# Kernel optimization log

Hardware: AMD Instinct MI355X
Metric: run time of the kernel (lower is better)

## Reference

```python
import jax, jax.numpy as jnp
import numpy as np
from jax import lax

WIN = 15      # sliding window size
BINS = 64     # luminance histogram bins
ALPHA = 0.9   # local vs global histogram mix
LAM1 = 0.5    # a-channel (material) removal weight
LAM2 = 0.5    # b-channel (material) removal weight
EPS = 1e-6


def _box_sum(x, win):
    return lax.reduce_window(x, 0.0, lax.add, (1, win, win, 1), (1, 1, 1, 1), 'SAME')


def setup_inputs() -> dict:
    key = jax.random.key(0)
    u = jax.random.uniform(key, (4, 3, 512, 512), dtype=jnp.float32)
    L = u[:, 0] * 100.0                 # L in [0,100]
    a = u[:, 1] * 255.0 - 128.0         # a in [-128,127]
    b = u[:, 2] * 255.0 - 128.0         # b in [-128,127]
    return {"batch_lab_raw": jnp.stack([L, a, b], axis=1)}


def reference(batch_lab_raw):
    # Normalize channels
    Ln = jnp.clip(batch_lab_raw[:, 0] / 100.0, 0.0, 1.0)      # (B,H,W)
    an = (batch_lab_raw[:, 1] + 128.0) / 255.0                # (B,H,W)
    bn = (batch_lab_raw[:, 2] + 128.0) / 255.0                # (B,H,W)

    # --- windowed luminance histogram anomaly ---
    idx = jnp.clip((Ln * BINS).astype(jnp.int32), 0, BINS - 1)            # (B,H,W)
    onehot = jax.nn.one_hot(idx, BINS, dtype=Ln.dtype)                    # (B,H,W,K)
    cnt = _box_sum(onehot, WIN)                                           # (B,H,W,K)
    n = _box_sum(jnp.ones(Ln.shape + (1,), Ln.dtype), WIN)                # (B,H,W,1) valid-pixel count
    # probability of own bin within local window
    p_loc = jnp.take_along_axis(cnt / n, idx[..., None], axis=-1)[..., 0]  # (B,H,W)
    # global per-image histogram probability of own bin
    p_glob_bins = jnp.mean(onehot, axis=(1, 2))                            # (B,K)
    p_glob = jnp.einsum('bhwk,bk->bhw', onehot, p_glob_bins)              # (B,H,W)

    S = -jnp.log(ALPHA * p_loc + (1.0 - ALPHA) * p_glob + EPS)            # surprise
    S_min = jnp.min(S, axis=(1, 2), keepdims=True)
    S_max = jnp.max(S, axis=(1, 2), keepdims=True)
    L_anom_norm = (S - S_min) / (S_max - S_min + EPS)                     # (B,H,W)

    # --- de-materialized illumination: remove local chroma (material) variation ---
    mu_a = _box_sum(an[..., None], WIN)[..., 0] / n[..., 0]
    mu_b = _box_sum(bn[..., None], WIN)[..., 0] / n[..., 0]
    L_perp = jnp.clip(Ln - LAM1 * (an - mu_a) - LAM2 * (bn - mu_b), 0.0, 1.0)

    return (L_perp[:, None], L_anom_norm[:, None])  # each (B,1,H,W)
```

## Files before the change

kernel.cpp:

```cpp
#include <hip/hip_runtime.h>

#define Hh 512
#define Ww 512
#define NPIX (Hh*Ww)
#define BATCH 4


__global__ __launch_bounds__(256) void k_hist(const float* __restrict__ in,
                                              unsigned* __restrict__ hp) {
    __shared__ unsigned lh[64];
    const int tid = threadIdx.x;
    if (tid < 64) lh[tid] = 0u;
    __syncthreads();
    const int img = blockIdx.x >> 6, sub = blockIdx.x & 63;
    const float4* Lp = (const float4*)(in + (size_t)img * 3 * NPIX) + sub * 1024;
    #pragma unroll
    for (int t = 0; t < 4; ++t) {
        float4 v = Lp[t*256 + tid];
        float f[4] = {v.x, v.y, v.z, v.w};
        #pragma unroll
        for (int j = 0; j < 4; ++j) {
            float ln = fminf(fmaxf(f[j] / 100.0f, 0.0f), 1.0f);
            int idx = min((int)(ln * 64.0f), 63);
            atomicAdd(&lh[idx], 1u);
        }
    }
    __syncthreads();
    if (tid < 64) hp[((size_t)img*64 + tid)*64 + sub] = lh[tid];
}

__global__ __launch_bounds__(256, 8) void k_main(const float* __restrict__ in,
        const unsigned* __restrict__ hp, float* __restrict__ bmin,
        float* __restrict__ bmax, float* __restrict__ out)
{
    __shared__ unsigned s_pk[46*9];
    __shared__ float s_c[46*36];
    __shared__ float s_cc[32*33];
    __shared__ float s_lnc[32*16];
    __shared__ float lhf[64];
    __shared__ float red[8];

    const int tx = threadIdx.x, ty = threadIdx.y;
    const int tid = ty*16 + tx;
    const int bx = blockIdx.x * 16, by = blockIdx.y * 32;
    const int img = blockIdx.z;
    const float* Lp = in + (size_t)img * 3 * NPIX;

    {
        const int bin = tid >> 2, grp = tid & 3;
        const uint4* p = (const uint4*)(hp + ((size_t)img*64 + bin)*64 + grp*16);
        uint4 x0 = p[0], x1 = p[1], x2 = p[2], x3 = p[3];
        unsigned sum = x0.x+x0.y+x0.z+x0.w + x1.x+x1.y+x1.z+x1.w
                     + x2.x+x2.y+x2.z+x2.w + x3.x+x3.y+x3.z+x3.w;
        sum += __shfl_xor(sum, 1);
        sum += __shfl_xor(sum, 2);
        if (grp == 0) lhf[bin] = (float)sum * (1.0f/262144.0f);
    }

    const int s = tx + 1;
    const int j0 = s >> 2;
    const unsigned m20 = 0x7FFFu << (s & 3);
    unsigned wm[5];
    #pragma unroll
    for (int i = 0; i < 5; ++i) {
        unsigned n = (m20 >> (4*i)) & 0xFu;
        wm[i] = (n&1u)*0x80u | (n&2u)*0x4000u | (n&4u)*0x200000u | (n&8u)*0x10000000u;
    }

    float4 Lv[2], Av[2], Bv[2];
    bool vld[2];
    #pragma unroll
    for (int it = 0; it < 2; ++it) {
        const int l = tid + it*256;
        const int r = l >> 3, c4 = l & 7;
        const int gy = by - 7 + r, gx0 = bx - 8 + c4*4;
        vld[it] = (l < 368) && gy >= 0 && gy < Hh && gx0 >= 0 && gx0 < Ww;
        if (vld[it]) {
            const int g = gy*Ww + gx0;
            Lv[it] = *(const float4*)(Lp + g);
            Av[it] = *(const float4*)(Lp + NPIX + g);
            Bv[it] = *(const float4*)(Lp + 2*NPIX + g);
        }
    }
    #pragma unroll
    for (int it = 0; it < 2; ++it) {
        const int l = tid + it*256;
        if (l < 368) {
            const int r = l >> 3, c4 = l & 7;
            unsigned pk = 0x7F7F7F7Fu;
            float4 cv = {0.f, 0.f, 0.f, 0.f};
            if (vld[it]) {
                const float l0 = fminf(fmaxf(Lv[it].x / 100.0f, 0.0f), 1.0f);
                const float l1 = fminf(fmaxf(Lv[it].y / 100.0f, 0.0f), 1.0f);
                const float l2 = fminf(fmaxf(Lv[it].z / 100.0f, 0.0f), 1.0f);
                const float l3 = fminf(fmaxf(Lv[it].w / 100.0f, 0.0f), 1.0f);
                const int b0 = min((int)(l0*64.0f), 63), b1 = min((int)(l1*64.0f), 63);
                const int b2 = min((int)(l2*64.0f), 63), b3 = min((int)(l3*64.0f), 63);
                pk = (unsigned)b0 | ((unsigned)b1<<8) | ((unsigned)b2<<16) | ((unsigned)b3<<24);
                const float k255 = 1.0f/255.0f;
                cv.x = (Av[it].x+128.0f)*k255 + (Bv[it].x+128.0f)*k255;
                cv.y = (Av[it].y+128.0f)*k255 + (Bv[it].y+128.0f)*k255;
                cv.z = (Av[it].z+128.0f)*k255 + (Bv[it].z+128.0f)*k255;
                cv.w = (Av[it].w+128.0f)*k255 + (Bv[it].w+128.0f)*k255;
                if (r >= 7 && r < 39 && c4 >= 2 && c4 <= 5) {
                    float4 lv4 = {l0, l1, l2, l3};
                    *(float4*)&s_lnc[(r-7)*16 + 4*(c4-2)] = lv4;
                }
            }
            s_pk[r*9 + c4] = pk;
            *(float4*)&s_c[r*36 + c4*4] = cv;
        }
    }
    __syncthreads();

    for (int l = tid; l < 512; l += 256) {
        const int q = l >> 5, c = l & 31;
        float mid = 0.f;
        #pragma unroll
        for (int k = 1; k < 15; ++k) mid += s_c[(2*q+k)*36 + c];
        s_cc[(2*q)*33 + c]   = mid + s_c[(2*q)*36 + c];
        s_cc[(2*q+1)*33 + c] = mid + s_c[(2*q+15)*36 + c];
    }
    __syncthreads();

    const int r0 = 2*ty;
    const int cbyte = tx + 8;
    const unsigned cb0 = (s_pk[(r0+7)*9 + (cbyte>>2)] >> (8*(cbyte&3))) & 0xFFu;
    const unsigned cb1 = (s_pk[(r0+8)*9 + (cbyte>>2)] >> (8*(cbyte&3))) & 0xFFu;
    const unsigned cb40 = cb0 * 0x01010101u;
    const unsigned cb41 = cb1 * 0x01010101u;
    const unsigned K = 0x7F7F7F7Fu;
    int a0 = 0, a1 = 0, a2 = 0, a3 = 0;
    const unsigned* rp = s_pk + r0*9 + j0;

    #pragma unroll
    for (int k = 0; k < 16; ++k) {
        const unsigned d0 = rp[k*9+0], d1 = rp[k*9+1], d2 = rp[k*9+2],
                       d3 = rp[k*9+3], d4 = rp[k*9+4];
        if (k != 15) {
            a0 += __popc(~((d0^cb40)+K) & wm[0]);
            a1 += __popc(~((d1^cb40)+K) & wm[1]);
            a0 += __popc(~((d2^cb40)+K) & wm[2]);
            a1 += __popc(~((d3^cb40)+K) & wm[3]);
            a0 += __popc(~((d4^cb40)+K) & wm[4]);
        }
        if (k != 0) {
            a2 += __popc(~((d0^cb41)+K) & wm[0]);
            a3 += __popc(~((d1^cb41)+K) & wm[1]);
            a2 += __popc(~((d2^cb41)+K) & wm[2]);
            a3 += __popc(~((d3^cb41)+K) & wm[3]);
            a2 += __popc(~((d4^cb41)+K) & wm[4]);
        }
    }
    const int c0 = a0 + a1, c1 = a2 + a3;

    float sc0 = 0.f, sc1 = 0.f;
    const float* ccp = s_cc + r0*33 + s;
    #pragma unroll
    for (int dx = 0; dx < 15; ++dx) { sc0 += ccp[dx]; sc1 += ccp[33+dx]; }

    const int gx = bx + tx;
    const int gy0 = by + r0;
    const int cols  = min(gx+7, Ww-1) - max(gx-7, 0) + 1;
    const int rows0 = min(gy0+7, Hh-1) - max(gy0-7, 0) + 1;
    const int rows1 = min(gy0+8, Hh-1) - max(gy0-6, 0) + 1;
    const float inv0 = __builtin_amdgcn_rcpf((float)(rows0*cols));
    const float inv1 = __builtin_amdgcn_rcpf((float)(rows1*cols));
    const float pg0 = lhf[cb0];
    const float pg1 = lhf[cb1];
    const float S0 = -__logf(0.9f*((float)c0*inv0) + 0.1f*pg0 + 1e-6f);
    const float S1 = -__logf(0.9f*((float)c1*inv1) + 0.1f*pg1 + 1e-6f);
    const int gbase = img*NPIX + gy0*Ww + gx;

    const float lp0 = s_lnc[r0*16 + tx]     - 0.5f*(s_c[(r0+7)*36 + tx+8] - sc0*inv0);
    const float lp1 = s_lnc[(r0+1)*16 + tx] - 0.5f*(s_c[(r0+8)*36 + tx+8] - sc1*inv1);
    out[gbase]      = fminf(fmaxf(lp0, 0.f), 1.f);
    out[gbase + Ww] = fminf(fmaxf(lp1, 0.f), 1.f);
    float* outN = out + (size_t)BATCH*NPIX;
    outN[gbase]      = S0;
    outN[gbase + Ww] = S1;

    float smin = fminf(S0, S1), smax = fmaxf(S0, S1);
    #pragma unroll
    for (int off = 32; off >= 1; off >>= 1) {
        smin = fminf(smin, __shfl_xor(smin, off));
        smax = fmaxf(smax, __shfl_xor(smax, off));
    }
    const int wid = tid >> 6;
    if ((tid & 63) == 0) { red[wid] = smin; red[4+wid] = smax; }
    __syncthreads();
    if (tid == 0) {
        const int bid = blockIdx.y*32 + blockIdx.x;
        bmin[img*512 + bid] = fminf(fminf(red[0],red[1]), fminf(red[2],red[3]));
        bmax[img*512 + bid] = fmaxf(fmaxf(red[4],red[5]), fmaxf(red[6],red[7]));
    }
}

__global__ __launch_bounds__(256) void k_norm(float* __restrict__ outN,
        const float* __restrict__ bmin, const float* __restrict__ bmax) {
    __shared__ float red[8];
    const int tid = threadIdx.x;
    const int img = blockIdx.x >> 8;

    float mn = __builtin_inff(), mx = -__builtin_inff();
    if (tid < 128) {
        float4 a = ((const float4*)(bmin + img*512))[tid];
        float4 b = ((const float4*)(bmax + img*512))[tid];
        mn = fminf(fminf(a.x, a.y), fminf(a.z, a.w));
        mx = fmaxf(fmaxf(b.x, b.y), fmaxf(b.z, b.w));
    }
    #pragma unroll
    for (int off = 32; off >= 1; off >>= 1) {
        mn = fminf(mn, __shfl_xor(mn, off));
        mx = fmaxf(mx, __shfl_xor(mx, off));
    }
    if ((tid & 63) == 0) { red[tid>>6] = mn; red[4 + (tid>>6)] = mx; }
    __syncthreads();
    const float vmin = fminf(fminf(red[0],red[1]), fminf(red[2],red[3]));
    const float vmax = fmaxf(fmaxf(red[4],red[5]), fmaxf(red[6],red[7]));
    const float inv = 1.0f / (vmax - vmin + 1e-6f);

    float4* p = (float4*)outN + (size_t)blockIdx.x*256;
    float4 v = p[tid];
    v.x = (v.x - vmin) * inv; v.y = (v.y - vmin) * inv;
    v.z = (v.z - vmin) * inv; v.w = (v.w - vmin) * inv;
    p[tid] = v;
}

extern "C" void kernel_launch(void* const* d_in, const int* in_sizes, int n_in,
                              void* d_out, int out_size, void* d_ws, size_t ws_size,
                              hipStream_t stream) {
    const float* in = (const float*)d_in[0];
    float* out = (float*)d_out;
    float* bmin = (float*)d_ws;
    float* bmax = bmin + BATCH*512;
    unsigned* hp = (unsigned*)(bmax + BATCH*512);

    k_hist<<<BATCH*64, 256, 0, stream>>>(in, hp);
    dim3 grid(Ww/16, Hh/32, BATCH), blk(16, 16);
    k_main<<<grid, blk, 0, stream>>>(in, hp, bmin, bmax, out);
    k_norm<<<BATCH*256, 256, 0, stream>>>(out + (size_t)BATCH*NPIX, bmin, bmax);
}
```

Baseline: 83.94 us.

## Grow main tile to 16x64 with four rows per thread and sliding column sums

Doubles the per-block tile height so each thread produces four output rows instead of two. This cuts halo reload overhead from 46/32 to 78/64 rows and amortizes the column-chroma sums, which now use a running add/subtract over eight rows. The extra per-thread work and larger shared-memory footprint lower the occupancy target from 8 to 4 blocks, and the grid drops to half as many blocks. The partial min/max buffers and the normalization reduction are resized to match.

```diff
diff --git a/kernel.cpp b/kernel.cpp
--- a/kernel.cpp
+++ b/kernel.cpp
@@ -29,20 +29,20 @@
     if (tid < 64) hp[((size_t)img*64 + tid)*64 + sub] = lh[tid];
 }
 
-__global__ __launch_bounds__(256, 8) void k_main(const float* __restrict__ in,
+__global__ __launch_bounds__(256, 4) void k_main(const float* __restrict__ in,
         const unsigned* __restrict__ hp, float* __restrict__ bmin,
         float* __restrict__ bmax, float* __restrict__ out)
 {
-    __shared__ unsigned s_pk[46*9];
-    __shared__ float s_c[46*36];
-    __shared__ float s_cc[32*33];
-    __shared__ float s_lnc[32*16];
+    __shared__ unsigned s_pk[78*9];
+    __shared__ float s_c[78*36];
+    __shared__ float s_cc[64*33];
+    __shared__ float s_lnc[64*16];
     __shared__ float lhf[64];
     __shared__ float red[8];
 
     const int tx = threadIdx.x, ty = threadIdx.y;
     const int tid = ty*16 + tx;
-    const int bx = blockIdx.x * 16, by = blockIdx.y * 32;
+    const int bx = blockIdx.x * 16, by = blockIdx.y * 64;
     const int img = blockIdx.z;
     const float* Lp = in + (size_t)img * 3 * NPIX;
 
@@ -67,14 +67,14 @@
         wm[i] = (n&1u)*0x80u | (n&2u)*0x4000u | (n&4u)*0x200000u | (n&8u)*0x10000000u;
     }
 
-    float4 Lv[2], Av[2], Bv[2];
-    bool vld[2];
-    #pragma unroll
-    for (int it = 0; it < 2; ++it) {
+    float4 Lv[3], Av[3], Bv[3];
+    bool vld[3];
+    #pragma unroll
+    for (int it = 0; it < 3; ++it) {
         const int l = tid + it*256;
         const int r = l >> 3, c4 = l & 7;
         const int gy = by - 7 + r, gx0 = bx - 8 + c4*4;
-        vld[it] = (l < 368) && gy >= 0 && gy < Hh && gx0 >= 0 && gx0 < Ww;
+        vld[it] = (l < 624) && gy >= 0 && gy < Hh && gx0 >= 0 && gx0 < Ww;
         if (vld[it]) {
             const int g = gy*Ww + gx0;
             Lv[it] = *(const float4*)(Lp + g);
@@ -83,9 +83,9 @@
         }
     }
     #pragma unroll
-    for (int it = 0; it < 2; ++it) {
+    for (int it = 0; it < 3; ++it) {
         const int l = tid + it*256;
-        if (l < 368) {
+        if (l < 624) {
             const int r = l >> 3, c4 = l & 7;
             unsigned pk = 0x7F7F7F7Fu;
             float4 cv = {0.f, 0.f, 0.f, 0.f};
@@ -102,7 +102,7 @@
                 cv.y = (Av[it].y+128.0f)*k255 + (Bv[it].y+128.0f)*k255;
                 cv.z = (Av[it].z+128.0f)*k255 + (Bv[it].z+128.0f)*k255;
                 cv.w = (Av[it].w+128.0f)*k255 + (Bv[it].w+128.0f)*k255;
-                if (r >= 7 && r < 39 && c4 >= 2 && c4 <= 5) {
+                if (r >= 7 && r < 71 && c4 >= 2 && c4 <= 5) {
                     float4 lv4 = {l0, l1, l2, l3};
                     *(float4*)&s_lnc[(r-7)*16 + 4*(c4-2)] = lv4;
                 }
@@ -113,74 +113,76 @@
     }
     __syncthreads();
 
-    for (int l = tid; l < 512; l += 256) {
-        const int q = l >> 5, c = l & 31;
-        float mid = 0.f;
-        #pragma unroll
-        for (int k = 1; k < 15; ++k) mid += s_c[(2*q+k)*36 + c];
-        s_cc[(2*q)*33 + c]   = mid + s_c[(2*q)*36 + c];
-        s_cc[(2*q+1)*33 + c] = mid + s_c[(2*q+15)*36 + c];
-    }
-    __syncthreads();
-
-    const int r0 = 2*ty;
-    const int cbyte = tx + 8;
-    const unsigned cb0 = (s_pk[(r0+7)*9 + (cbyte>>2)] >> (8*(cbyte&3))) & 0xFFu;
-    const unsigned cb1 = (s_pk[(r0+8)*9 + (cbyte>>2)] >> (8*(cbyte&3))) & 0xFFu;
-    const unsigned cb40 = cb0 * 0x01010101u;
-    const unsigned cb41 = cb1 * 0x01010101u;
+    if (tid < 248) {
+        const int grp = tid / 31;
+        const int col = tid - grp*31;
+        const int r0v = grp*8;
+        float sum = 0.f;
+        #pragma unroll
+        for (int k = 0; k < 15; ++k) sum += s_c[(r0v+k)*36 + col];
+        s_cc[r0v*33 + col] = sum;
+        #pragma unroll
+        for (int jj = 1; jj < 8; ++jj) {
+            sum += s_c[(r0v+14+jj)*36 + col] - s_c[(r0v+jj-1)*36 + col];
+            s_cc[(r0v+jj)*33 + col] = sum;
+        }
+    }
+    __syncthreads();
+
+    const int r0 = 4*ty;
+    const int cb_dw = (tx+8) >> 2, cb_sh = 8*((tx+8)&3);
+    unsigned cbb[4], cb4[4];
+    #pragma unroll
+    for (int j = 0; j < 4; ++j) {
+        cbb[j] = (s_pk[(r0+7+j)*9 + cb_dw] >> cb_sh) & 0xFFu;
+        cb4[j] = cbb[j] * 0x01010101u;
+    }
     const unsigned K = 0x7F7F7F7Fu;
-    int a0 = 0, a1 = 0, a2 = 0, a3 = 0;
+    int acc[4] = {0,0,0,0};
     const unsigned* rp = s_pk + r0*9 + j0;
 
     #pragma unroll
-    for (int k = 0; k < 16; ++k) {
+    for (int k = 0; k < 18; ++k) {
         const unsigned d0 = rp[k*9+0], d1 = rp[k*9+1], d2 = rp[k*9+2],
                        d3 = rp[k*9+3], d4 = rp[k*9+4];
-        if (k != 15) {
-            a0 += __popc(~((d0^cb40)+K) & wm[0]);
-            a1 += __popc(~((d1^cb40)+K) & wm[1]);
-            a0 += __popc(~((d2^cb40)+K) & wm[2]);
-            a1 += __popc(~((d3^cb40)+K) & wm[3]);
-            a0 += __popc(~((d4^cb40)+K) & wm[4]);
-        }
-        if (k != 0) {
-            a2 += __popc(~((d0^cb41)+K) & wm[0]);
-            a3 += __popc(~((d1^cb41)+K) & wm[1]);
-            a2 += __popc(~((d2^cb41)+K) & wm[2]);
-            a3 += __popc(~((d3^cb41)+K) & wm[3]);
-            a2 += __popc(~((d4^cb41)+K) & wm[4]);
-        }
-    }
-    const int c0 = a0 + a1, c1 = a2 + a3;
-
-    float sc0 = 0.f, sc1 = 0.f;
-    const float* ccp = s_cc + r0*33 + s;
-    #pragma unroll
-    for (int dx = 0; dx < 15; ++dx) { sc0 += ccp[dx]; sc1 += ccp[33+dx]; }
+        #pragma unroll
+        for (int j = 0; j < 4; ++j) {
+            if (j <= k && k <= j + 14) {
+                acc[j] += __popc(~((d0^cb4[j])+K) & wm[0]);
+                acc[j] += __popc(~((d1^cb4[j])+K) & wm[1]);
+                acc[j] += __popc(~((d2^cb4[j])+K) & wm[2]);
+                acc[j] += __popc(~((d3^cb4[j])+K) & wm[3]);
+                acc[j] += __popc(~((d4^cb4[j])+K) & wm[4]);
+            }
+        }
+    }
+
+    float sc[4] = {0.f, 0.f, 0.f, 0.f};
+    #pragma unroll
+    for (int j = 0; j < 4; ++j) {
+        const float* ccp = s_cc + (r0+j)*33 + s;
+        #pragma unroll
+        for (int dx = 0; dx < 15; ++dx) sc[j] += ccp[dx];
+    }
 
     const int gx = bx + tx;
-    const int gy0 = by + r0;
-    const int cols  = min(gx+7, Ww-1) - max(gx-7, 0) + 1;
-    const int rows0 = min(gy0+7, Hh-1) - max(gy0-7, 0) + 1;
-    const int rows1 = min(gy0+8, Hh-1) - max(gy0-6, 0) + 1;
-    const float inv0 = __builtin_amdgcn_rcpf((float)(rows0*cols));
-    const float inv1 = __builtin_amdgcn_rcpf((float)(rows1*cols));
-    const float pg0 = lhf[cb0];
-    const float pg1 = lhf[cb1];
-    const float S0 = -__logf(0.9f*((float)c0*inv0) + 0.1f*pg0 + 1e-6f);
-    const float S1 = -__logf(0.9f*((float)c1*inv1) + 0.1f*pg1 + 1e-6f);
-    const int gbase = img*NPIX + gy0*Ww + gx;
-
-    const float lp0 = s_lnc[r0*16 + tx]     - 0.5f*(s_c[(r0+7)*36 + tx+8] - sc0*inv0);
-    const float lp1 = s_lnc[(r0+1)*16 + tx] - 0.5f*(s_c[(r0+8)*36 + tx+8] - sc1*inv1);
-    out[gbase]      = fminf(fmaxf(lp0, 0.f), 1.f);
-    out[gbase + Ww] = fminf(fmaxf(lp1, 0.f), 1.f);
+    const int cols = min(gx+7, Ww-1) - max(gx-7, 0) + 1;
     float* outN = out + (size_t)BATCH*NPIX;
-    outN[gbase]      = S0;
-    outN[gbase + Ww] = S1;
-
-    float smin = fminf(S0, S1), smax = fmaxf(S0, S1);
+    float smin = __builtin_inff(), smax = -__builtin_inff();
+    #pragma unroll
+    for (int j = 0; j < 4; ++j) {
+        const int gy = by + r0 + j;
+        const int rows = min(gy+7, Hh-1) - max(gy-7, 0) + 1;
+        const float invn = __builtin_amdgcn_rcpf((float)(rows*cols));
+        const float S = -__logf(0.9f*((float)acc[j]*invn) + 0.1f*lhf[cbb[j]] + 1e-6f);
+        const int gbase = img*NPIX + gy*Ww + gx;
+        outN[gbase] = S;
+        const float lp = s_lnc[(r0+j)*16 + tx]
+                       - 0.5f*(s_c[(r0+7+j)*36 + tx+8] - sc[j]*invn);
+        out[gbase] = fminf(fmaxf(lp, 0.f), 1.f);
+        smin = fminf(smin, S); smax = fmaxf(smax, S);
+    }
+
     #pragma unroll
     for (int off = 32; off >= 1; off >>= 1) {
         smin = fminf(smin, __shfl_xor(smin, off));
@@ -191,34 +193,32 @@
     __syncthreads();
     if (tid == 0) {
         const int bid = blockIdx.y*32 + blockIdx.x;
-        bmin[img*512 + bid] = fminf(fminf(red[0],red[1]), fminf(red[2],red[3]));
-        bmax[img*512 + bid] = fmaxf(fmaxf(red[4],red[5]), fmaxf(red[6],red[7]));
+        bmin[img*256 + bid] = fminf(fminf(red[0],red[1]), fminf(red[2],red[3]));
+        bmax[img*256 + bid] = fmaxf(fmaxf(red[4],red[5]), fmaxf(red[6],red[7]));
     }
 }
 
 __global__ __launch_bounds__(256) void k_norm(float* __restrict__ outN,
         const float* __restrict__ bmin, const float* __restrict__ bmax) {
-    __shared__ float red[8];
+    __shared__ float red[2];
     const int tid = threadIdx.x;
     const int img = blockIdx.x >> 8;
 
-    float mn = __builtin_inff(), mx = -__builtin_inff();
-    if (tid < 128) {
-        float4 a = ((const float4*)(bmin + img*512))[tid];
-        float4 b = ((const float4*)(bmax + img*512))[tid];
-        mn = fminf(fminf(a.x, a.y), fminf(a.z, a.w));
-        mx = fmaxf(fmaxf(b.x, b.y), fmaxf(b.z, b.w));
-    }
-    #pragma unroll
-    for (int off = 32; off >= 1; off >>= 1) {
-        mn = fminf(mn, __shfl_xor(mn, off));
-        mx = fmaxf(mx, __shfl_xor(mx, off));
-    }
-    if ((tid & 63) == 0) { red[tid>>6] = mn; red[4 + (tid>>6)] = mx; }
-    __syncthreads();
-    const float vmin = fminf(fminf(red[0],red[1]), fminf(red[2],red[3]));
-    const float vmax = fmaxf(fmaxf(red[4],red[5]), fmaxf(red[6],red[7]));
-    const float inv = 1.0f / (vmax - vmin + 1e-6f);
+    if (tid < 64) {
+        float4 a = ((const float4*)(bmin + img*256))[tid];
+        float4 b = ((const float4*)(bmax + img*256))[tid];
+        float mn = fminf(fminf(a.x, a.y), fminf(a.z, a.w));
+        float mx = fmaxf(fmaxf(b.x, b.y), fmaxf(b.z, b.w));
+        #pragma unroll
+        for (int off = 32; off >= 1; off >>= 1) {
+            mn = fminf(mn, __shfl_xor(mn, off));
+            mx = fmaxf(mx, __shfl_xor(mx, off));
+        }
+        if (tid == 0) { red[0] = mn; red[1] = mx; }
+    }
+    __syncthreads();
+    const float vmin = red[0];
+    const float inv = 1.0f / (red[1] - vmin + 1e-6f);
 
     float4* p = (float4*)outN + (size_t)blockIdx.x*256;
     float4 v = p[tid];
@@ -233,11 +233,11 @@
     const float* in = (const float*)d_in[0];
     float* out = (float*)d_out;
     float* bmin = (float*)d_ws;
-    float* bmax = bmin + BATCH*512;
-    unsigned* hp = (unsigned*)(bmax + BATCH*512);
+    float* bmax = bmin + BATCH*256;
+    unsigned* hp = (unsigned*)(bmax + BATCH*256);
 
     k_hist<<<BATCH*64, 256, 0, stream>>>(in, hp);
-    dim3 grid(Ww/16, Hh/32, BATCH), blk(16, 16);
+    dim3 grid(Ww/16, Hh/64, BATCH), blk(16, 16);
     k_main<<<grid, blk, 0, stream>>>(in, hp, bmin, bmax, out);
     k_norm<<<BATCH*256, 256, 0, stream>>>(out + (size_t)BATCH*NPIX, bmin, bmax);
 }
```

Result: slower. 86.69 us (+3.3%).
